# Optimization experiments

Hardware: AMD Instinct MI355X
Metric: run time of the kernel (lower is better)

## Reference

```python
import jax, jax.numpy as jnp
import numpy as np

CR = 4; D = 768; H = 12; DH = 64; L = 3; I = 3072
W1S = 128  # one-sided sliding window = config.attention_window(256) // 2 (transformers convention)
MAXPOS = 7200; MLP = 512; NCLS = 3
EPS = 1e-12

def layer_norm(x, s, b):
    m = jnp.mean(x, -1, keepdims=True)
    v = jnp.var(x, -1, keepdims=True)
    return (x - m) * jax.lax.rsqrt(v + EPS) * s + b

def band_attention(q, k, v, w):
    # q,k,v: [B,H,S,dh]; each token attends to +-w neighbors (Longformer sliding chunks, no global tokens)
    B, Hh, S, dh = q.shape
    nc = S // w
    qc = q.reshape(B, Hh, nc, w, dh)
    kp = jnp.pad(k, ((0, 0), (0, 0), (w, w), (0, 0)))
    vp = jnp.pad(v, ((0, 0), (0, 0), (w, w), (0, 0)))
    idx = jnp.arange(nc)[:, None] * w + jnp.arange(3 * w)[None, :]          # [nc, 3w]
    kc = kp[:, :, idx]                                                      # [B,H,nc,3w,dh]
    vc = vp[:, :, idx]
    scores = jnp.einsum('bhcqd,bhckd->bhcqk', qc, kc) / np.float32(np.sqrt(dh))
    rel = jnp.arange(3 * w)[None, :] - w - jnp.arange(w)[:, None]           # [w,3w] key_pos - query_pos
    kpos = jnp.arange(nc)[:, None, None] * w + jnp.arange(3 * w)[None, None, :] - w
    mask = (jnp.abs(rel)[None] <= w) & (kpos >= 0) & (kpos < S)             # [nc,w,3w]
    scores = jnp.where(mask[None, None], scores, jnp.float32(-1e9))
    probs = jax.nn.softmax(scores, axis=-1)
    out = jnp.einsum('bhcqk,bhckd->bhcqd', probs, vc)
    return out.reshape(B, Hh, S, dh)

def forward(x, proj_w, proj_b, pos_emb, tok_emb, emb_ln_s, emb_ln_b,
            wq, bq, wk, bk, wv, bv, wo, bo, ln1_s, ln1_b,
            wi, bi, wo2, bo2, ln2_s, ln2_b,
            pool_w, pool_b, head_ln_s, head_ln_b, head_w1, head_b1, head_w2, head_b2):
    n, c, t, wd, hh = x.shape
    tc, sc = t // CR, wd // CR
    # torch unfold(dim, size, step) with size==step == contiguous block reshape
    xr = x[:, :, :tc * CR].reshape(n, c, CR, tc, CR, sc, CR, sc)
    xr = xr.transpose(0, 1, 2, 4, 6, 3, 5, 7)            # n,c,cr_t,cr_w,cr_h,tc,sc,sc
    xr = xr.reshape(n, c, CR ** 3, tc * sc * sc)
    xr = xr.transpose(0, 3, 2, 1).reshape(n, tc * sc * sc, CR ** 3 * c)
    h = xr @ proj_w + proj_b                             # [B,S,D]
    B, S = h.shape[0], h.shape[1]
    pos_ids = jnp.arange(S) % (MAXPOS - 2)               # no padding: S is already a multiple of 2w
    h = h + pos_emb[pos_ids][None] + tok_emb[0][None, None]
    h = layer_norm(h, emb_ln_s, emb_ln_b)
    for l in range(L):
        q = (h @ wq[l] + bq[l]).reshape(B, S, H, DH).transpose(0, 2, 1, 3)
        k = (h @ wk[l] + bk[l]).reshape(B, S, H, DH).transpose(0, 2, 1, 3)
        v = (h @ wv[l] + bv[l]).reshape(B, S, H, DH).transpose(0, 2, 1, 3)
        a = band_attention(q, k, v, W1S).transpose(0, 2, 1, 3).reshape(B, S, D)
        h = layer_norm(h + a @ wo[l] + bo[l], ln1_s[l], ln1_b[l])
        f = jax.nn.gelu(h @ wi[l] + bi[l], approximate=False) @ wo2[l] + bo2[l]
        h = layer_norm(h + f, ln2_s[l], ln2_b[l])
    pooled = jnp.tanh(h[:, 0] @ pool_w + pool_b)         # LongformerPooler on first token
    z = layer_norm(pooled, head_ln_s, head_ln_b)
    z = jax.nn.gelu(z @ head_w1 + head_b1, approximate=False)
    return z @ head_w2 + head_b2                         # [B, num_classes]

def setup_inputs() -> dict:
    key = jax.random.key(0)
    ks = iter(jax.random.split(key, 40))
    p = lambda *s: jax.random.normal(next(ks), s, jnp.float32) * 0.02
    d = {
        'x': jax.random.normal(next(ks), (8, 3, 64, 32, 32), jnp.float32),
        'position_ids': jnp.tile(jnp.arange(1024, dtype=jnp.int32)[None], (8, 1)),
        'proj_w': p(3 * CR ** 3, D), 'proj_b': p(D),
        'pos_emb': p(MAXPOS, D), 'tok_emb': p(2, D),
        'emb_ln_s': jnp.ones((D,), jnp.float32), 'emb_ln_b': jnp.zeros((D,), jnp.float32),
        'wq': p(L, D, D), 'bq': p(L, D), 'wk': p(L, D, D), 'bk': p(L, D),
        'wv': p(L, D, D), 'bv': p(L, D), 'wo': p(L, D, D), 'bo': p(L, D),
        'ln1_s': jnp.ones((L, D), jnp.float32), 'ln1_b': jnp.zeros((L, D), jnp.float32),
        'wi': p(L, D, I), 'bi': p(L, I), 'wo2': p(L, I, D), 'bo2': p(L, D),
        'ln2_s': jnp.ones((L, D), jnp.float32), 'ln2_b': jnp.zeros((L, D), jnp.float32),
        'pool_w': p(D, D), 'pool_b': p(D),
        'head_ln_s': jnp.ones((D,), jnp.float32), 'head_ln_b': jnp.zeros((D,), jnp.float32),
        'head_w1': p(D, MLP), 'head_b1': p(MLP),
        'head_w2': p(MLP, NCLS), 'head_b2': p(NCLS),
    }
    return d

def reference(x, position_ids, proj_w, proj_b, pos_emb, tok_emb, emb_ln_s, emb_ln_b,
              wq, bq, wk, bk, wv, bv, wo, bo, ln1_s, ln1_b,
              wi, bi, wo2, bo2, ln2_s, ln2_b,
              pool_w, pool_b, head_ln_s, head_ln_b, head_w1, head_b1, head_w2, head_b2):
    # position_ids is overwritten inside the spat_temp branch of the original forward (arange over cuboids)
    return forward(x, proj_w, proj_b, pos_emb, tok_emb, emb_ln_s, emb_ln_b,
                   wq, bq, wk, bk, wv, bv, wo, bo, ln1_s, ln1_b,
                   wi, bi, wo2, bo2, ln2_s, ln2_b,
                   pool_w, pool_b, head_ln_s, head_ln_b, head_w1, head_b1, head_w2, head_b2)
```

## Files before the change

kernel.cpp:

```cpp
#include <hip/hip_runtime.h>
#include <hip/hip_bf16.h>
#include <math.h>


typedef __attribute__((ext_vector_type(8))) short short8;
typedef __attribute__((ext_vector_type(4))) short short4v;
typedef __attribute__((ext_vector_type(4))) float floatx4;

__device__ __forceinline__ float gelu_exact(float x) {
    float ax = fabsf(x) * 0.70710678118654752440f;
    float t  = 1.f / (1.f + 0.3275911f * ax);
    float y  = t * (0.254829592f + t * (-0.284496736f + t * (1.421413741f +
               t * (-1.453152027f + t * 1.061405429f))));
    float erfv = copysignf(1.f - y * __expf(-ax * ax), x);
    return 0.5f * x * (1.f + erfv);
}

__device__ __forceinline__ short bfs(float x) {
    __hip_bfloat16 h = __float2bfloat16(x);
    short s;
    __builtin_memcpy(&s, &h, 2);
    return s;
}

__device__ __forceinline__ float bf2f(short s) {
    unsigned u = ((unsigned)(unsigned short)s) << 16;
    float f;
    __builtin_memcpy(&f, &u, 4);
    return f;
}

#define GLOAD_LDS16(g, l) __builtin_amdgcn_global_load_lds( \
    (const __attribute__((address_space(1))) void*)(g),     \
    (__attribute__((address_space(3))) void*)(l), 16, 0, 0)

__global__ __launch_bounds__(256) void transpose_bf16(
    const float* __restrict__ W, __hip_bfloat16* __restrict__ Wt,
    int K, int N, long inLS, long outLS)
{
    __shared__ float tile[32][33];
    int l = blockIdx.z;
    const float* Wl = W + (long)l * inLS;
    __hip_bfloat16* Wtl = Wt + (long)l * outLS;
    int lx = threadIdx.x & 31, ly = threadIdx.x >> 5;
    int kb = blockIdx.y * 32, nb = blockIdx.x * 32;
    #pragma unroll
    for (int r = 0; r < 32; r += 8)
        tile[ly + r][lx] = Wl[(long)(kb + ly + r) * N + nb + lx];
    __syncthreads();
    #pragma unroll
    for (int r = 0; r < 32; r += 8)
        Wtl[(long)(nb + ly + r) * K + kb + lx] = __float2bfloat16(tile[lx][ly + r]);
}

__global__ void pack_qkv_bias(const float* __restrict__ bq,
                              const float* __restrict__ bk,
                              const float* __restrict__ bv,
                              float* __restrict__ out)
{
    int l = blockIdx.x, tid = threadIdx.x;
    out[l * 2304 + tid]        = bq[l * 768 + tid];
    out[l * 2304 + 768 + tid]  = bk[l * 768 + tid];
    out[l * 2304 + 1536 + tid] = bv[l * 768 + tid];
}

__global__ __launch_bounds__(192) void gather_x(
    const float* __restrict__ x, __hip_bfloat16* __restrict__ xr)
{
    int tok = blockIdx.x;
    int b = tok >> 10, s = tok & 1023;
    int tci = s >> 6, sci = (s >> 3) & 7, scj = s & 7;
    int f = threadIdx.x;
    int ch  = f % 3;
    int crc = f / 3;
    int cr1 = crc >> 4, cr2 = (crc >> 2) & 3, cr3 = crc & 3;
    float v = x[(((b * 3 + ch) * 64) + cr1 * 16 + tci) * 1024 +
                (cr2 * 8 + sci) * 32 + cr3 * 8 + scj];
    xr[(long)tok * 192 + f] = __float2bfloat16(v);
}

template<int ACT>
__global__ __launch_bounds__(256) void mfma_gemm(
    const __hip_bfloat16* __restrict__ A, const __hip_bfloat16* __restrict__ Bt,
    const float* __restrict__ bias, __hip_bfloat16* __restrict__ C,
    int M, int N, int K)
{
    __shared__ short lds_raw[16384];
    __hip_bfloat16* As = (__hip_bfloat16*)lds_raw;
    __hip_bfloat16* Bs = As + 8192;
    int tid  = threadIdx.x;
    int wave = tid >> 6, lane = tid & 63;
    int L = blockIdx.x;
    long m0 = (long)(L & 63) * 128, n0 = (long)(L >> 6) * 128;
    int wr = wave >> 1, wc = wave & 1;
    floatx4 acc[4][4] = {};

    int srow = (wave * 128 + lane) >> 2;
    int sch  = (lane & 3) ^ ((lane >> 3) & 3);
    const __hip_bfloat16* Ag = A  + (m0 + srow) * K + sch * 8;
    const __hip_bfloat16* Bg = Bt + (n0 + srow) * K + sch * 8;
    int lm = lane & 15, lg = lane >> 4;
    int lk8 = ((lg ^ ((lm >> 1) & 3))) * 8;

    auto stage = [&](int buf, int k0) {
        __hip_bfloat16* a = As + buf * 4096 + wave * 1024;
        __hip_bfloat16* b = Bs + buf * 4096 + wave * 1024;
        GLOAD_LDS16(Ag + k0,          a);
        GLOAD_LDS16(Ag + 16 * K + k0, a + 512);
        GLOAD_LDS16(Bg + k0,          b);
        GLOAD_LDS16(Bg + 16 * K + k0, b + 512);
    };

    stage(0, 0);
    int buf = 0;
    for (int k0 = 0; k0 < K; k0 += 32, buf ^= 1) {
        __syncthreads();
        if (k0 + 32 < K) stage(buf ^ 1, k0 + 32);
        const __hip_bfloat16* Ab = As + buf * 4096;
        const __hip_bfloat16* Bb = Bs + buf * 4096;
        short8 af[4], bf4[4];
        #pragma unroll
        for (int mi = 0; mi < 4; mi++)
            af[mi] = *(const short8*)&Ab[(wr * 64 + mi * 16 + lm) * 32 + lk8];
        #pragma unroll
        for (int ni = 0; ni < 4; ni++)
            bf4[ni] = *(const short8*)&Bb[(wc * 64 + ni * 16 + lm) * 32 + lk8];
        #pragma unroll
        for (int mi = 0; mi < 4; mi++)
            #pragma unroll
            for (int ni = 0; ni < 4; ni++)
                acc[mi][ni] = __builtin_amdgcn_mfma_f32_16x16x32_bf16(
                    af[mi], bf4[ni], acc[mi][ni], 0, 0, 0);
    }
    __syncthreads();

    float bvv[4];
    #pragma unroll
    for (int ni = 0; ni < 4; ni++)
        bvv[ni] = bias[n0 + wc * 64 + ni * 16 + lm];
    int erow = tid >> 4;
    int ecol = (tid & 15) * 8;
    #pragma unroll
    for (int p = 0; p < 2; p++) {
        if (wr == p) {
            #pragma unroll
            for (int mi = 0; mi < 4; mi++)
                #pragma unroll
                for (int ni = 0; ni < 4; ni++)
                    #pragma unroll
                    for (int j = 0; j < 4; j++) {
                        float o = acc[mi][ni][j] + bvv[ni];
                        if (ACT == 1) o = gelu_exact(o);
                        lds_raw[(mi * 16 + lg * 4 + j) * 136 +
                                wc * 64 + ni * 16 + lm] = bfs(o);
                    }
        }
        __syncthreads();
        #pragma unroll
        for (int rr = 0; rr < 4; rr++) {
            int r = erow + rr * 16;
            short8 v = *(const short8*)&lds_raw[r * 136 + ecol];
            *(short8*)&C[(m0 + p * 64 + r) * N + n0 + ecol] = v;
        }
        __syncthreads();
    }
}

__global__ __launch_bounds__(192) void pos_ln_kernel(
    const __hip_bfloat16* __restrict__ t, const float* __restrict__ pos_emb,
    const float* __restrict__ tok_emb, const float* __restrict__ ln_s,
    const float* __restrict__ ln_b, float* __restrict__ h,
    __hip_bfloat16* __restrict__ hbf)
{
    int tok = blockIdx.x;
    int s = tok & 1023;
    int tid = threadIdx.x;
    int d = tid * 4;
    __shared__ float red[6];
    short4v tv = *(const short4v*)&t[(long)tok * 768 + d];
    float4 pv = *(const float4*)&pos_emb[s * 768 + d];
    float4 kv = *(const float4*)&tok_emb[d];
    float a[4] = { bf2f(tv[0]) + pv.x + kv.x, bf2f(tv[1]) + pv.y + kv.y,
                   bf2f(tv[2]) + pv.z + kv.z, bf2f(tv[3]) + pv.w + kv.w };
    float sum = a[0] + a[1] + a[2] + a[3];
    float sumsq = a[0]*a[0] + a[1]*a[1] + a[2]*a[2] + a[3]*a[3];
    #pragma unroll
    for (int off = 32; off; off >>= 1) {
        sum   += __shfl_down(sum, off, 64);
        sumsq += __shfl_down(sumsq, off, 64);
    }
    if ((tid & 63) == 0) { red[tid >> 6] = sum; red[3 + (tid >> 6)] = sumsq; }
    __syncthreads();
    sum   = red[0] + red[1] + red[2];
    sumsq = red[3] + red[4] + red[5];
    float mean = sum * (1.f / 768.f);
    float var  = sumsq * (1.f / 768.f) - mean * mean;
    float rs   = rsqrtf(var + 1e-12f);
    float4 sv = *(const float4*)&ln_s[d];
    float4 bv = *(const float4*)&ln_b[d];
    float4 o;
    o.x = (a[0] - mean) * rs * sv.x + bv.x;
    o.y = (a[1] - mean) * rs * sv.y + bv.y;
    o.z = (a[2] - mean) * rs * sv.z + bv.z;
    o.w = (a[3] - mean) * rs * sv.w + bv.w;
    *(float4*)&h[(long)tok * 768 + d] = o;
    short4v ob = { bfs(o.x), bfs(o.y), bfs(o.z), bfs(o.w) };
    *(short4v*)&hbf[(long)tok * 768 + d] = ob;
}

__global__ __launch_bounds__(256) void attn_kernel(
    const __hip_bfloat16* __restrict__ QKV, __hip_bfloat16* __restrict__ Ob)
{
    __shared__ __hip_bfloat16 KV[128 * 72];
    __shared__ __hip_bfloat16 Pl[4][32 * 136];
    __shared__ float alpha_s[4][32];
    __shared__ float l_s[4][32];

    int blk = blockIdx.x;
    int ci = blk & 7, hh = (blk >> 3) % 12, b = blk / 96;
    int tid = threadIdx.x, w = tid >> 6, lane = tid & 63;
    int lm = lane & 15, lg = lane >> 4;
    __hip_bfloat16* Pw = &Pl[w][0];

    short8 qf[2][2];
    #pragma unroll
    for (int nt = 0; nt < 2; nt++) {
        int q = ci * 128 + w * 32 + nt * 16 + lm;
        const __hip_bfloat16* qp = &QKV[((long)(b * 1024 + q)) * 2304 + hh * 64];
        #pragma unroll
        for (int ks = 0; ks < 2; ks++)
            qf[nt][ks] = *(const short8*)(qp + ks * 32 + lg * 8);
    }

    floatx4 accO[2][4] = {};
    float m_run[2] = {-1e30f, -1e30f};
    float l_run[2] = {0.f, 0.f};

    for (int tt = 0; tt < 3; tt++) {
        __syncthreads();
        #pragma unroll
        for (int i = 0; i < 4; i++) {
            int e = tid + i * 256;
            int jj = e >> 3, dd = (e & 7) * 8;
            int kpos = ci * 128 + tt * 128 + jj - 128;
            short8 kv = {};
            if (kpos >= 0 && kpos < 1024)
                kv = *(const short8*)&QKV[((long)(b * 1024 + kpos)) * 2304 + 768 + hh * 64 + dd];
            *(short8*)&KV[jj * 72 + dd] = kv;
        }
        __syncthreads();

        floatx4 accS[8][2] = {};
        #pragma unroll
        for (int ks = 0; ks < 2; ks++)
            #pragma unroll
            for (int mt = 0; mt < 8; mt++) {
                short8 kf = *(const short8*)&KV[(mt * 16 + lm) * 72 + ks * 32 + lg * 8];
                accS[mt][0] = __builtin_amdgcn_mfma_f32_16x16x32_bf16(kf, qf[0][ks], accS[mt][0], 0, 0, 0);
                accS[mt][1] = __builtin_amdgcn_mfma_f32_16x16x32_bf16(kf, qf[1][ks], accS[mt][1], 0, 0, 0);
            }

        float tmax[2] = {-1e30f, -1e30f};
        #pragma unroll
        for (int nt = 0; nt < 2; nt++) {
            int r = w * 32 + nt * 16 + lm;
            #pragma unroll
            for (int mt = 0; mt < 8; mt++)
                #pragma unroll
                for (int j = 0; j < 4; j++) {
                    int jrel = tt * 128 + mt * 16 + lg * 4 + j;
                    int kpos = ci * 128 + jrel - 128;
                    bool valid = (jrel >= r) && (jrel <= r + 256) &&
                                 (kpos >= 0) && (kpos < 1024);
                    float s = valid ? accS[mt][nt][j] * 0.125f : -1e9f;
                    accS[mt][nt][j] = s;
                    tmax[nt] = fmaxf(tmax[nt], s);
                }
            tmax[nt] = fmaxf(tmax[nt], __shfl_xor(tmax[nt], 16));
            tmax[nt] = fmaxf(tmax[nt], __shfl_xor(tmax[nt], 32));
        }

        float al[2];
        #pragma unroll
        for (int nt = 0; nt < 2; nt++) {
            float mnew = fmaxf(m_run[nt], tmax[nt]);
            al[nt] = __expf(m_run[nt] - mnew);
            m_run[nt] = mnew;
            float ts = 0.f;
            #pragma unroll
            for (int mt = 0; mt < 8; mt++) {
                short4v pp;
                #pragma unroll
                for (int j = 0; j < 4; j++) {
                    float p = __expf(accS[mt][nt][j] - mnew);
                    ts += p;
                    pp[j] = bfs(p);
                }
                *(short4v*)&Pw[(nt * 16 + lm) * 136 + mt * 16 + lg * 4] = pp;
            }
            ts += __shfl_xor(ts, 16);
            ts += __shfl_xor(ts, 32);
            l_run[nt] = l_run[nt] * al[nt] + ts;
        }
        if (lg < 2) alpha_s[w][lg * 16 + lm] = al[lg];

        __syncthreads();
        #pragma unroll
        for (int i = 0; i < 4; i++) {
            int e = tid + i * 256;
            int jj = e >> 3, dd = (e & 7) * 8;
            int kpos = ci * 128 + tt * 128 + jj - 128;
            short8 vv = {};
            if (kpos >= 0 && kpos < 1024)
                vv = *(const short8*)&QKV[((long)(b * 1024 + kpos)) * 2304 + 1536 + hh * 64 + dd];
            short* kvs = (short*)KV;
            #pragma unroll
            for (int m2 = 0; m2 < 8; m2++)
                kvs[(dd + m2) * 136 + jj] = vv[m2];
        }
        __syncthreads();

        #pragma unroll
        for (int mo = 0; mo < 2; mo++)
            #pragma unroll
            for (int j = 0; j < 4; j++) {
                float a = alpha_s[w][mo * 16 + lg * 4 + j];
                #pragma unroll
                for (int nd = 0; nd < 4; nd++)
                    accO[mo][nd][j] *= a;
            }

        #pragma unroll
        for (int kk = 0; kk < 4; kk++) {
            short8 pf[2], vf[4];
            #pragma unroll
            for (int mo = 0; mo < 2; mo++)
                pf[mo] = *(const short8*)&Pw[(mo * 16 + lm) * 136 + kk * 32 + lg * 8];
            #pragma unroll
            for (int nd = 0; nd < 4; nd++)
                vf[nd] = *(const short8*)&KV[(nd * 16 + lm) * 136 + kk * 32 + lg * 8];
            #pragma unroll
            for (int mo = 0; mo < 2; mo++)
                #pragma unroll
                for (int nd = 0; nd < 4; nd++)
                    accO[mo][nd] = __builtin_amdgcn_mfma_f32_16x16x32_bf16(
                        pf[mo], vf[nd], accO[mo][nd], 0, 0, 0);
        }
    }

    if (lg < 2) l_s[w][lg * 16 + lm] = l_run[lg];
    #pragma unroll
    for (int mo = 0; mo < 2; mo++)
        #pragma unroll
        for (int j = 0; j < 4; j++) {
            int qr = mo * 16 + lg * 4 + j;
            float rl = 1.f / l_s[w][qr];
            int q  = w * 32 + qr;
            long base = ((long)(b * 1024 + ci * 128 + q)) * 768 + hh * 64;
            #pragma unroll
            for (int nd = 0; nd < 4; nd++)
                Ob[base + nd * 16 + lm] = __float2bfloat16(accO[mo][nd][j] * rl);
        }
}

__global__ __launch_bounds__(192) void add_ln_kernel(
    float* __restrict__ h, const __hip_bfloat16* __restrict__ t,
    const float* __restrict__ ln_s, const float* __restrict__ ln_b,
    __hip_bfloat16* __restrict__ hbf)
{
    int tok = blockIdx.x;
    int tid = threadIdx.x;
    int d = tid * 4;
    __shared__ float red[6];
    float* hrow = &h[(long)tok * 768];
    float4 hv = *(const float4*)&hrow[d];
    short4v tv = *(const short4v*)&t[(long)tok * 768 + d];
    float a[4] = { hv.x + bf2f(tv[0]), hv.y + bf2f(tv[1]),
                   hv.z + bf2f(tv[2]), hv.w + bf2f(tv[3]) };
    float sum = a[0] + a[1] + a[2] + a[3];
    float sumsq = a[0]*a[0] + a[1]*a[1] + a[2]*a[2] + a[3]*a[3];
    #pragma unroll
    for (int off = 32; off; off >>= 1) {
        sum   += __shfl_down(sum, off, 64);
        sumsq += __shfl_down(sumsq, off, 64);
    }
    if ((tid & 63) == 0) { red[tid >> 6] = sum; red[3 + (tid >> 6)] = sumsq; }
    __syncthreads();
    sum   = red[0] + red[1] + red[2];
    sumsq = red[3] + red[4] + red[5];
    float mean = sum * (1.f / 768.f);
    float var  = sumsq * (1.f / 768.f) - mean * mean;
    float rs   = rsqrtf(var + 1e-12f);
    float4 sv = *(const float4*)&ln_s[d];
    float4 bv = *(const float4*)&ln_b[d];
    float4 o;
    o.x = (a[0] - mean) * rs * sv.x + bv.x;
    o.y = (a[1] - mean) * rs * sv.y + bv.y;
    o.z = (a[2] - mean) * rs * sv.z + bv.z;
    o.w = (a[3] - mean) * rs * sv.w + bv.w;
    *(float4*)&hrow[d] = o;
    short4v ob = { bfs(o.x), bfs(o.y), bfs(o.z), bfs(o.w) };
    *(short4v*)&hbf[(long)tok * 768 + d] = ob;
}

__global__ __launch_bounds__(256) void pool_split(
    const __hip_bfloat16* __restrict__ hbf, const __hip_bfloat16* __restrict__ pool_wt,
    const float* __restrict__ pool_b, float* __restrict__ pooled)
{
    int g = blockIdx.x * 256 + threadIdx.x;
    int out = g >> 3, t8 = g & 7;
    int b = out / 768, d = out - b * 768;
    const __hip_bfloat16* hr = hbf + (long)b * 1024 * 768;
    const __hip_bfloat16* wr = pool_wt + (long)d * 768;
    float acc = 0.f;
    #pragma unroll
    for (int kk = 0; kk < 96; kk += 8) {
        int k = t8 * 96 + kk;
        short8 hv = *(const short8*)&hr[k];
        short8 wv = *(const short8*)&wr[k];
        #pragma unroll
        for (int j = 0; j < 8; j++) acc += bf2f(hv[j]) * bf2f(wv[j]);
    }
    acc += __shfl_down(acc, 4, 64);
    acc += __shfl_down(acc, 2, 64);
    acc += __shfl_down(acc, 1, 64);
    if (t8 == 0) pooled[out] = tanhf(acc + pool_b[d]);
}

__global__ __launch_bounds__(256) void ln_z_kernel(
    const float* __restrict__ pooled, const float* __restrict__ hln_s,
    const float* __restrict__ hln_b, __hip_bfloat16* __restrict__ zbf)
{
    int b = blockIdx.x, tid = threadIdx.x;
    __shared__ float red[8];
    const float* pr = &pooled[b * 768];
    float p0 = pr[tid], p1 = pr[tid + 256], p2 = pr[tid + 512];
    float sum = p0 + p1 + p2;
    float sumsq = p0 * p0 + p1 * p1 + p2 * p2;
    #pragma unroll
    for (int off = 32; off; off >>= 1) {
        sum   += __shfl_down(sum, off, 64);
        sumsq += __shfl_down(sumsq, off, 64);
    }
    if ((tid & 63) == 0) { red[tid >> 6] = sum; red[4 + (tid >> 6)] = sumsq; }
    __syncthreads();
    sum   = red[0] + red[1] + red[2] + red[3];
    sumsq = red[4] + red[5] + red[6] + red[7];
    float mean = sum * (1.f / 768.f);
    float var  = sumsq * (1.f / 768.f) - mean * mean;
    float rs   = rsqrtf(var + 1e-12f);
    zbf[b * 768 + tid]       = __float2bfloat16((p0 - mean) * rs * hln_s[tid]       + hln_b[tid]);
    zbf[b * 768 + tid + 256] = __float2bfloat16((p1 - mean) * rs * hln_s[tid + 256] + hln_b[tid + 256]);
    zbf[b * 768 + tid + 512] = __float2bfloat16((p2 - mean) * rs * hln_s[tid + 512] + hln_b[tid + 512]);
}

__global__ __launch_bounds__(256) void mlp_split(
    const __hip_bfloat16* __restrict__ zbf, const __hip_bfloat16* __restrict__ w1t,
    const float* __restrict__ b1, float* __restrict__ z1)
{
    int g = blockIdx.x * 256 + threadIdx.x;
    int out = g >> 3, t8 = g & 7;
    int b = out >> 9, d = out & 511;
    const __hip_bfloat16* zr = zbf + b * 768;
    const __hip_bfloat16* wr = w1t + (long)d * 768;
    float acc = 0.f;
    #pragma unroll
    for (int kk = 0; kk < 96; kk += 8) {
        int k = t8 * 96 + kk;
        short8 zv = *(const short8*)&zr[k];
        short8 wv = *(const short8*)&wr[k];
        #pragma unroll
        for (int j = 0; j < 8; j++) acc += bf2f(zv[j]) * bf2f(wv[j]);
    }
    acc += __shfl_down(acc, 4, 64);
    acc += __shfl_down(acc, 2, 64);
    acc += __shfl_down(acc, 1, 64);
    if (t8 == 0) z1[out] = gelu_exact(acc + b1[d]);
}

__global__ __launch_bounds__(256) void head_final_kernel(
    const float* __restrict__ z1, const float* __restrict__ w2,
    const float* __restrict__ b2, float* __restrict__ out)
{
    int tid = threadIdx.x;
    int g = tid >> 3, t8 = tid & 7;
    if (g < 24) {
        int b = g / 3, o = g % 3;
        float acc = 0.f;
        for (int k = t8; k < 512; k += 8)
            acc += z1[b * 512 + k] * w2[k * 3 + o];
        acc += __shfl_down(acc, 4, 64);
        acc += __shfl_down(acc, 2, 64);
        acc += __shfl_down(acc, 1, 64);
        if (t8 == 0) out[b * 3 + o] = acc + b2[o];
    }
}

extern "C" void kernel_launch(void* const* d_in, const int* in_sizes, int n_in,
                              void* d_out, int out_size, void* d_ws, size_t ws_size,
                              hipStream_t stream) {
    const float* x       = (const float*)d_in[0];
    const float* proj_w  = (const float*)d_in[2];
    const float* proj_b  = (const float*)d_in[3];
    const float* pos_emb = (const float*)d_in[4];
    const float* tok_emb = (const float*)d_in[5];
    const float* eln_s   = (const float*)d_in[6];
    const float* eln_b   = (const float*)d_in[7];
    const float* wq      = (const float*)d_in[8];
    const float* bq      = (const float*)d_in[9];
    const float* wk      = (const float*)d_in[10];
    const float* bk      = (const float*)d_in[11];
    const float* wv      = (const float*)d_in[12];
    const float* bv      = (const float*)d_in[13];
    const float* wo      = (const float*)d_in[14];
    const float* bo      = (const float*)d_in[15];
    const float* ln1_s   = (const float*)d_in[16];
    const float* ln1_b   = (const float*)d_in[17];
    const float* wi      = (const float*)d_in[18];
    const float* bi      = (const float*)d_in[19];
    const float* wo2     = (const float*)d_in[20];
    const float* bo2     = (const float*)d_in[21];
    const float* ln2_s   = (const float*)d_in[22];
    const float* ln2_b   = (const float*)d_in[23];
    const float* pool_w  = (const float*)d_in[24];
    const float* pool_b  = (const float*)d_in[25];
    const float* hln_s   = (const float*)d_in[26];
    const float* hln_b   = (const float*)d_in[27];
    const float* hw1     = (const float*)d_in[28];
    const float* hb1     = (const float*)d_in[29];
    const float* hw2     = (const float*)d_in[30];
    const float* hb2     = (const float*)d_in[31];

    char* wp = (char*)d_ws;
    auto alloc = [&](size_t bytes) {
        char* p = wp; wp += (bytes + 255) & ~(size_t)255; return p;
    };
    float*          h       = (float*)alloc(8192ll * 768 * 4);
    __hip_bfloat16* qkv_bf  = (__hip_bfloat16*)alloc(8192ll * 2304 * 2);
    __hip_bfloat16* t_bf    = (__hip_bfloat16*)alloc(8192ll * 768 * 2);
    __hip_bfloat16* mlp_bf  = (__hip_bfloat16*)alloc(8192ll * 3072 * 2);
    __hip_bfloat16* h_bf    = (__hip_bfloat16*)alloc(8192ll * 768 * 2);
    __hip_bfloat16* a_bf    = (__hip_bfloat16*)alloc(8192ll * 768 * 2);
    __hip_bfloat16* qkvw_t  = (__hip_bfloat16*)alloc(3ll * 2304 * 768 * 2);
    __hip_bfloat16* wo_t    = (__hip_bfloat16*)alloc(3ll * 768 * 768 * 2);
    __hip_bfloat16* wi_t    = (__hip_bfloat16*)alloc(3ll * 3072 * 768 * 2);
    __hip_bfloat16* wo2_t   = (__hip_bfloat16*)alloc(3ll * 768 * 3072 * 2);
    float*          qkv_b   = (float*)alloc(3ll * 2304 * 4);
    __hip_bfloat16* xr_bf   = (__hip_bfloat16*)alloc(8192ll * 192 * 2);
    __hip_bfloat16* projw_t = (__hip_bfloat16*)alloc(768ll * 192 * 2);
    __hip_bfloat16* poolw_t = (__hip_bfloat16*)alloc(768ll * 768 * 2);
    __hip_bfloat16* w1_t    = (__hip_bfloat16*)alloc(512ll * 768 * 2);
    float*          pooled  = (float*)alloc(8ll * 768 * 4);
    __hip_bfloat16* z_bf    = (__hip_bfloat16*)alloc(8ll * 768 * 2);
    float*          z1      = (float*)alloc(8ll * 512 * 4);

    transpose_bf16<<<dim3(24, 24, 3), 256, 0, stream>>>(wq, qkvw_t,               768, 768,  768ll * 768,  2304ll * 768);
    transpose_bf16<<<dim3(24, 24, 3), 256, 0, stream>>>(wk, qkvw_t + 768 * 768,   768, 768,  768ll * 768,  2304ll * 768);
    transpose_bf16<<<dim3(24, 24, 3), 256, 0, stream>>>(wv, qkvw_t + 1536 * 768,  768, 768,  768ll * 768,  2304ll * 768);
    transpose_bf16<<<dim3(24, 24, 3), 256, 0, stream>>>(wo, wo_t,                 768, 768,  768ll * 768,  768ll * 768);
    transpose_bf16<<<dim3(96, 24, 3), 256, 0, stream>>>(wi, wi_t,                 768, 3072, 768ll * 3072, 3072ll * 768);
    transpose_bf16<<<dim3(24, 96, 3), 256, 0, stream>>>(wo2, wo2_t,               3072, 768, 3072ll * 768, 768ll * 3072);
    transpose_bf16<<<dim3(24, 6, 1),  256, 0, stream>>>(proj_w, projw_t,          192, 768,  0, 0);
    transpose_bf16<<<dim3(24, 24, 1), 256, 0, stream>>>(pool_w, poolw_t,          768, 768,  0, 0);
    transpose_bf16<<<dim3(16, 24, 1), 256, 0, stream>>>(hw1, w1_t,                768, 512,  0, 0);
    pack_qkv_bias<<<3, 768, 0, stream>>>(bq, bk, bv, qkv_b);

    gather_x<<<8192, 192, 0, stream>>>(x, xr_bf);
    mfma_gemm<0><<<6 * 64, 256, 0, stream>>>(
        xr_bf, projw_t, proj_b, t_bf, 8192, 768, 192);
    pos_ln_kernel<<<8192, 192, 0, stream>>>(t_bf, pos_emb, tok_emb, eln_s, eln_b, h, h_bf);

    for (int l = 0; l < 3; l++) {
        mfma_gemm<0><<<18 * 64, 256, 0, stream>>>(
            h_bf, qkvw_t + (long)l * 2304 * 768, qkv_b + l * 2304, qkv_bf,
            8192, 2304, 768);
        attn_kernel<<<768, 256, 0, stream>>>(qkv_bf, a_bf);
        mfma_gemm<0><<<6 * 64, 256, 0, stream>>>(
            a_bf, wo_t + (long)l * 768 * 768, bo + l * 768, t_bf,
            8192, 768, 768);
        add_ln_kernel<<<8192, 192, 0, stream>>>(h, t_bf, ln1_s + l * 768, ln1_b + l * 768, h_bf);
        mfma_gemm<1><<<24 * 64, 256, 0, stream>>>(
            h_bf, wi_t + (long)l * 3072 * 768, bi + l * 3072, mlp_bf,
            8192, 3072, 768);
        mfma_gemm<0><<<6 * 64, 256, 0, stream>>>(
            mlp_bf, wo2_t + (long)l * 768 * 3072, bo2 + l * 768, t_bf,
            8192, 768, 3072);
        add_ln_kernel<<<8192, 192, 0, stream>>>(h, t_bf, ln2_s + l * 768, ln2_b + l * 768, h_bf);
    }

    pool_split<<<192, 256, 0, stream>>>(h_bf, poolw_t, pool_b, pooled);
    ln_z_kernel<<<8, 256, 0, stream>>>(pooled, hln_s, hln_b, z_bf);
    mlp_split<<<128, 256, 0, stream>>>(z_bf, w1_t, hb1, z1);
    head_final_kernel<<<1, 256, 0, stream>>>(z1, hw2, hb2, (float*)d_out);
}
```

Measured before the change: 1.088 ms.

## Triple-buffer GEMM LDS staging with explicit waitcnt barriers and MFMA priority

Switches the bf16 MFMA GEMM from double to triple LDS buffering, prefetching two K-tiles ahead. __syncthreads is replaced by raw s_barrier plus hand-placed vmcnt/lgkmcnt waits, and s_setprio is raised around the MFMA block, so global loads can overlap compute more deeply. LDS use grows by half, which can lower occupancy, and correctness now depends on the manual wait counts being right.

```diff
diff --git a/kernel.cpp b/kernel.cpp
--- a/kernel.cpp
+++ b/kernel.cpp
@@ -85,9 +85,8 @@
     const float* __restrict__ bias, __hip_bfloat16* __restrict__ C,
     int M, int N, int K)
 {
-    __shared__ short lds_raw[16384];
-    __hip_bfloat16* As = (__hip_bfloat16*)lds_raw;
-    __hip_bfloat16* Bs = As + 8192;
+    __shared__ short lds_raw[24576];
+    __hip_bfloat16* LB = (__hip_bfloat16*)lds_raw;
     int tid  = threadIdx.x;
     int wave = tid >> 6, lane = tid & 63;
     int L = blockIdx.x;
@@ -103,21 +102,29 @@
     int lk8 = ((lg ^ ((lm >> 1) & 3))) * 8;
 
     auto stage = [&](int buf, int k0) {
-        __hip_bfloat16* a = As + buf * 4096 + wave * 1024;
-        __hip_bfloat16* b = Bs + buf * 4096 + wave * 1024;
+        __hip_bfloat16* a = LB + buf * 8192 + wave * 1024;
+        __hip_bfloat16* b = a + 4096;
         GLOAD_LDS16(Ag + k0,          a);
         GLOAD_LDS16(Ag + 16 * K + k0, a + 512);
         GLOAD_LDS16(Bg + k0,          b);
         GLOAD_LDS16(Bg + 16 * K + k0, b + 512);
     };
 
+    int NT = K >> 5;
     stage(0, 0);
-    int buf = 0;
-    for (int k0 = 0; k0 < K; k0 += 32, buf ^= 1) {
-        __syncthreads();
-        if (k0 + 32 < K) stage(buf ^ 1, k0 + 32);
-        const __hip_bfloat16* Ab = As + buf * 4096;
-        const __hip_bfloat16* Bb = Bs + buf * 4096;
+    if (NT > 1) {
+        stage(1, 32);
+        asm volatile("s_waitcnt vmcnt(4)" ::: "memory");
+    } else {
+        asm volatile("s_waitcnt vmcnt(0)" ::: "memory");
+    }
+    __builtin_amdgcn_s_barrier();
+
+    int c0 = 0, c1 = 1, c2 = 2;
+    for (int t = 0; t < NT; ++t) {
+        if (t + 2 < NT) stage(c2, (t + 2) << 5);
+        const __hip_bfloat16* Ab = LB + c0 * 8192;
+        const __hip_bfloat16* Bb = Ab + 4096;
         short8 af[4], bf4[4];
         #pragma unroll
         for (int mi = 0; mi < 4; mi++)
@@ -125,12 +132,21 @@
         #pragma unroll
         for (int ni = 0; ni < 4; ni++)
             bf4[ni] = *(const short8*)&Bb[(wc * 64 + ni * 16 + lm) * 32 + lk8];
+        __builtin_amdgcn_s_barrier();
+        asm volatile("s_waitcnt lgkmcnt(0)" ::: "memory");
+        __builtin_amdgcn_sched_barrier(0);
+        __builtin_amdgcn_s_setprio(1);
         #pragma unroll
         for (int mi = 0; mi < 4; mi++)
             #pragma unroll
             for (int ni = 0; ni < 4; ni++)
                 acc[mi][ni] = __builtin_amdgcn_mfma_f32_16x16x32_bf16(
                     af[mi], bf4[ni], acc[mi][ni], 0, 0, 0);
+        __builtin_amdgcn_s_setprio(0);
+        if (t + 2 < NT) asm volatile("s_waitcnt vmcnt(4)" ::: "memory");
+        else            asm volatile("s_waitcnt vmcnt(0)" ::: "memory");
+        __builtin_amdgcn_s_barrier();
+        int tr_ = c0; c0 = c1; c1 = c2; c2 = tr_;
     }
     __syncthreads();
 
```

Measured after the change: 1.087 ms. No clear change (-0.1%).

## Load GEMM B operand directly from global into registers, halving LDS use

Applied to the files above, without the earlier changes.

The GEMM now stages only the A tile through LDS. Each wave reads its B fragments straight from global memory into registers with a two-register-set ping-pong, and the k-loop is unrolled by two. LDS per block roughly halves and launch bounds request three blocks per CU, aiming for higher occupancy and less LDS traffic. In exchange, B is no longer shared across waves, so global and L2 traffic rises, register pressure grows, and K must be a multiple of 64.

```diff
diff --git a/kernel.cpp b/kernel.cpp
--- a/kernel.cpp
+++ b/kernel.cpp
@@ -80,14 +80,13 @@
 }
 
 template<int ACT>
-__global__ __launch_bounds__(256) void mfma_gemm(
+__global__ __launch_bounds__(256, 3) void mfma_gemm(
     const __hip_bfloat16* __restrict__ A, const __hip_bfloat16* __restrict__ Bt,
     const float* __restrict__ bias, __hip_bfloat16* __restrict__ C,
     int M, int N, int K)
 {
-    __shared__ short lds_raw[16384];
+    __shared__ short lds_raw[8704];
     __hip_bfloat16* As = (__hip_bfloat16*)lds_raw;
-    __hip_bfloat16* Bs = As + 8192;
     int tid  = threadIdx.x;
     int wave = tid >> 6, lane = tid & 63;
     int L = blockIdx.x;
@@ -97,40 +96,65 @@
 
     int srow = (wave * 128 + lane) >> 2;
     int sch  = (lane & 3) ^ ((lane >> 3) & 3);
-    const __hip_bfloat16* Ag = A  + (m0 + srow) * K + sch * 8;
-    const __hip_bfloat16* Bg = Bt + (n0 + srow) * K + sch * 8;
+    const __hip_bfloat16* Ag = A + (m0 + srow) * K + sch * 8;
     int lm = lane & 15, lg = lane >> 4;
     int lk8 = ((lg ^ ((lm >> 1) & 3))) * 8;
 
+    const __hip_bfloat16* Bg0 = Bt + (n0 + wc * 64 + lm) * (long)K + lg * 8;
+    long nK16 = (long)16 * K;
+
     auto stage = [&](int buf, int k0) {
         __hip_bfloat16* a = As + buf * 4096 + wave * 1024;
-        __hip_bfloat16* b = Bs + buf * 4096 + wave * 1024;
         GLOAD_LDS16(Ag + k0,          a);
         GLOAD_LDS16(Ag + 16 * K + k0, a + 512);
-        GLOAD_LDS16(Bg + k0,          b);
-        GLOAD_LDS16(Bg + 16 * K + k0, b + 512);
     };
-
+    auto loadB = [&](short8* bf, int k0) {
+        #pragma unroll
+        for (int ni = 0; ni < 4; ni++)
+            bf[ni] = *(const short8*)(Bg0 + ni * nK16 + k0);
+    };
+
+    short8 bfA[4], bfB[4];
     stage(0, 0);
+    loadB(bfA, 0);
     int buf = 0;
-    for (int k0 = 0; k0 < K; k0 += 32, buf ^= 1) {
-        __syncthreads();
-        if (k0 + 32 < K) stage(buf ^ 1, k0 + 32);
-        const __hip_bfloat16* Ab = As + buf * 4096;
-        const __hip_bfloat16* Bb = Bs + buf * 4096;
-        short8 af[4], bf4[4];
-        #pragma unroll
-        for (int mi = 0; mi < 4; mi++)
-            af[mi] = *(const short8*)&Ab[(wr * 64 + mi * 16 + lm) * 32 + lk8];
-        #pragma unroll
-        for (int ni = 0; ni < 4; ni++)
-            bf4[ni] = *(const short8*)&Bb[(wc * 64 + ni * 16 + lm) * 32 + lk8];
-        #pragma unroll
-        for (int mi = 0; mi < 4; mi++)
+    for (int k0 = 0; k0 < K; k0 += 64) {
+        __syncthreads();
+        stage(buf ^ 1, k0 + 32);
+        loadB(bfB, k0 + 32);
+        {
+            const __hip_bfloat16* Ab = As + buf * 4096;
+            short8 af[4];
+            #pragma unroll
+            for (int mi = 0; mi < 4; mi++)
+                af[mi] = *(const short8*)&Ab[(wr * 64 + mi * 16 + lm) * 32 + lk8];
             #pragma unroll
             for (int ni = 0; ni < 4; ni++)
-                acc[mi][ni] = __builtin_amdgcn_mfma_f32_16x16x32_bf16(
-                    af[mi], bf4[ni], acc[mi][ni], 0, 0, 0);
+                #pragma unroll
+                for (int mi = 0; mi < 4; mi++)
+                    acc[mi][ni] = __builtin_amdgcn_mfma_f32_16x16x32_bf16(
+                        af[mi], bfA[ni], acc[mi][ni], 0, 0, 0);
+        }
+        buf ^= 1;
+        __syncthreads();
+        if (k0 + 64 < K) {
+            stage(buf ^ 1, k0 + 64);
+            loadB(bfA, k0 + 64);
+        }
+        {
+            const __hip_bfloat16* Ab = As + buf * 4096;
+            short8 af[4];
+            #pragma unroll
+            for (int mi = 0; mi < 4; mi++)
+                af[mi] = *(const short8*)&Ab[(wr * 64 + mi * 16 + lm) * 32 + lk8];
+            #pragma unroll
+            for (int ni = 0; ni < 4; ni++)
+                #pragma unroll
+                for (int mi = 0; mi < 4; mi++)
+                    acc[mi][ni] = __builtin_amdgcn_mfma_f32_16x16x32_bf16(
+                        af[mi], bfB[ni], acc[mi][ni], 0, 0, 0);
+        }
+        buf ^= 1;
     }
     __syncthreads();
 
```

New measurement: 1.439 ms. 32.3% more time.
